# Performance work log

Hardware: AMD Instinct MI355X
Metric: run time of the kernel (lower is better)

The kernel has to match this reference:

```python
import jax, jax.numpy as jnp
import numpy as np

B, S, E, P, K, H = 32, 512, 1024, 256, 3, 8
KERNELS = 4  # conv repeated KERNELS times then averaged -> identical to a single conv


def setup_inputs() -> dict:
    key = jax.random.key(0)
    ks = jax.random.split(key, 8)
    sc = 0.02
    x = jax.random.normal(ks[0], (B, S, E), jnp.float32)
    # lengths must satisfy 3 <= l <= S-1 so slice [1:l+1] and conv length l-2 are valid
    seq_length = jax.random.randint(ks[1], (B,), 16, S - 1)
    proj_w = jax.random.normal(ks[2], (E, P), jnp.float32) * sc
    proj_b = jnp.zeros((P,), jnp.float32)
    conv_w = jax.random.normal(ks[3], (P, P, K), jnp.float32) * sc  # (out, in, width)
    conv_b = jnp.zeros((P,), jnp.float32)
    attn_w = jax.random.normal(ks[4], (P, H * S), jnp.float32) * sc
    attn_b = jnp.zeros((H * S,), jnp.float32)
    c1_w = jax.random.normal(ks[5], (P, P // 2), jnp.float32) * sc
    c1_b = jnp.zeros((P // 2,), jnp.float32)
    c2_w = jax.random.normal(ks[6], (P // 2, 2), jnp.float32) * sc
    c2_b = jnp.zeros((2,), jnp.float32)
    return dict(x=x, seq_length=seq_length, proj_w=proj_w, proj_b=proj_b,
                conv_w=conv_w, conv_b=conv_b, attn_w=attn_w, attn_b=attn_b,
                c1_w=c1_w, c1_b=c1_b, c2_w=c2_w, c2_b=c2_b)


def _forward(x, seq_length, proj_w, proj_b, conv_w, conv_b, attn_w, attn_b,
             c1_w, c1_b, c2_w, c2_b):
    # projection: (B,S,E) -> (B,S,P)
    proj = jnp.einsum('bse,ep->bsp', x, proj_w) + proj_b
    proj_pc = jnp.transpose(proj, (0, 2, 1))  # (B,P,S)
    # original convs each sample over slice [1:l+1]; conv is local, so conv the
    # full slice [1:] once and mask invalid tail positions per sample.
    conv = jax.lax.conv_general_dilated(
        proj_pc[:, :, 1:], conv_w, window_strides=(1,), padding='VALID',
        dimension_numbers=('NCH', 'OIH', 'NCH'))  # (B,P,S-K)
    conv = jax.nn.relu(conv + conv_b[None, :, None])
    # sum of KERNELS identical relu(conv) outputs divided by KERNELS == conv (identity)
    m = S - K  # conv output length over slice [1:]
    l = seq_length[:, None]  # (B,1)
    valid = jnp.arange(m)[None, :] < (l - (K - 1))  # output j valid iff j < l-2
    conv = jnp.where(valid[:, None, :], conv, 0.0)
    # pad: position 0 zero, conv outputs at 1..l-2, zeros after -> (B,P,S)
    rep_conv = jnp.zeros((B, P, S), conv.dtype).at[:, :, 1:1 + m].set(conv)
    rep_conv = jnp.transpose(rep_conv, (0, 2, 1))  # (B,S,P)
    # attention: logits (B,S,H*S), softmax over the FULL H*S axis (original dim=1)
    logits = jnp.einsum('bsp,pk->bsk', rep_conv, attn_w) + attn_b
    attn = jax.nn.softmax(logits, axis=-1).reshape(B, S, H, S)
    # per sample: mean over heads, sum over query rows -> weights over key pos q
    w = attn.sum(axis=(1, 2)) / H  # (B,S)
    rep_attn = jnp.einsum('bq,bqp->bp', w, rep_conv)  # (B,P)
    h = jnp.einsum('bp,ph->bh', rep_attn, c1_w) + c1_b
    h = jnp.where(h > 0, h, 0.01 * h)  # LeakyReLU(0.01)
    cls = jnp.einsum('bh,hc->bc', h, c2_w) + c2_b
    return jax.nn.softmax(cls, axis=-1)


def reference(x, seq_length, proj_w, proj_b, conv_w, conv_b, attn_w, attn_b,
              c1_w, c1_b, c2_w, c2_b):
    probs = _forward(x, seq_length, proj_w, proj_b, conv_w, conv_b,
                     attn_w, attn_b, c1_w, c1_b, c2_w, c2_b)
    return probs, jnp.argmax(probs, axis=1)
```

## Files before the change

kernel.cpp:

```cpp
#include <hip/hip_runtime.h>

#define B_ 32
#define S_ 512
#define E_ 1024
#define P_ 256
#define HH 8

typedef __attribute__((ext_vector_type(8))) short bf16x8;
typedef __attribute__((ext_vector_type(8))) unsigned short us8;
typedef __attribute__((ext_vector_type(4))) unsigned short us4;
typedef __attribute__((ext_vector_type(16))) float f32x16;

static __device__ __forceinline__ unsigned short f2bf(float f) {
  union { float f; unsigned int u; } v;
  v.f = f;
  unsigned int r = (v.u + 0x7FFFu + ((v.u >> 16) & 1u)) >> 16;
  return (unsigned short)r;
}
static __device__ __forceinline__ float bf2f(unsigned short u) {
  union { unsigned int u; float f; } v;
  v.u = ((unsigned int)u) << 16;
  return v.f;
}

__global__ __launch_bounds__(256) void k_wtT(const float* __restrict__ cw,
                                             unsigned short* __restrict__ wtT) {
  int o = blockIdx.x, k = blockIdx.y, i = threadIdx.x;
  wtT[o * 768 + k * 256 + i] = f2bf(cw[o * 768 + i * 3 + k]);
}

__global__ __launch_bounds__(256) void k_pwT(const float* __restrict__ pw,
                                             unsigned short* __restrict__ pwT) {
  __shared__ float T[32][33];
  int n0 = blockIdx.x * 32;
  int k0 = blockIdx.y * 32;
  int tx = threadIdx.x & 31, ty = threadIdx.x >> 5;
#pragma unroll
  for (int i = 0; i < 4; i++)
    T[ty + i * 8][tx] = pw[(k0 + ty + i * 8) * P_ + n0 + tx];
  __syncthreads();
#pragma unroll
  for (int i = 0; i < 4; i++)
    pwT[(size_t)(n0 + ty + i * 8) * E_ + k0 + tx] = f2bf(T[tx][ty + i * 8]);
}

__global__ __launch_bounds__(256) void k_awT(const float* __restrict__ aw,
                                             unsigned short* __restrict__ awT) {
  __shared__ float T[32][33];
  int j0 = blockIdx.x * 32;
  int k0 = blockIdx.y * 32;
  int tx = threadIdx.x & 31, ty = threadIdx.x >> 5;
#pragma unroll
  for (int i = 0; i < 4; i++)
    T[ty + i * 8][tx] = aw[(k0 + ty + i * 8) * 4096 + j0 + tx];
  __syncthreads();
#pragma unroll
  for (int i = 0; i < 4; i++)
    awT[(size_t)(j0 + ty + i * 8) * 256 + k0 + tx] = f2bf(T[tx][ty + i * 8]);
}

__global__ __launch_bounds__(256) void k_swz(const unsigned short* __restrict__ src,
                                             unsigned short* __restrict__ dst,
                                             int K, int NK) {
  int g = blockIdx.x, kc = blockIdx.y * 4 + (threadIdx.x >> 6);
  int l = threadIdx.x & 63;
  us8 v = *(const us8*)(src + (size_t)(g * 32 + (l & 31)) * K + kc * 16 + (l >> 5) * 8);
  *(us8*)(dst + ((size_t)g * NK + kc) * 512 + l * 8) = v;
}

__global__ __launch_bounds__(256) void k_zero(float* __restrict__ p) {
  p[blockIdx.x * 256 + threadIdx.x] = 0.f;
}

__global__ __launch_bounds__(256) void k_proj_mfma(const float* __restrict__ x,
                                                   const unsigned short* __restrict__ pwB,
                                                   const float* __restrict__ pb,
                                                   unsigned short* __restrict__ proj16) {
  __shared__ unsigned short As[16 * 64 * 8];
  const int m0 = blockIdx.x * 64;
  const int t = threadIdx.x;
  const int w = t >> 6, lane = t & 63, ln31 = lane & 31, kh = lane >> 5;
  const int c0 = w * 64;

  f32x16 acc00, acc01, acc10, acc11;
#pragma unroll
  for (int r = 0; r < 16; r++) { acc00[r] = 0.f; acc01[r] = 0.f; acc10[r] = 0.f; acc11[r] = 0.f; }

  const unsigned short* bp0 = pwB + (size_t)(2 * w) * 64 * 512 + lane * 8;
  const unsigned short* bp1 = bp0 + (size_t)64 * 512;

  for (int kc = 0; kc < E_; kc += 128) {
#pragma unroll
    for (int i = 0; i < 8; i++) {
      int c = t + i * 256;
      int row = c >> 5, pos = c & 31;
      float4 v = *(const float4*)(x + (size_t)(m0 + row) * E_ + kc + pos * 4);
      us4 h;
      h[0] = f2bf(v.x); h[1] = f2bf(v.y); h[2] = f2bf(v.z); h[3] = f2bf(v.w);
      *(us4*)&As[((pos >> 1) * 64 + row) * 8 + (pos & 1) * 4] = h;
    }
    __syncthreads();
    const int kcs = kc >> 4;
#pragma unroll
    for (int kk = 0; kk < 8; kk++) {
      bf16x8 a0 = *(const bf16x8*)&As[((2 * kk + kh) * 64 + ln31) * 8];
      bf16x8 a1 = *(const bf16x8*)&As[((2 * kk + kh) * 64 + 32 + ln31) * 8];
      bf16x8 b0 = *(const bf16x8*)(bp0 + (size_t)(kcs + kk) * 512);
      bf16x8 b1 = *(const bf16x8*)(bp1 + (size_t)(kcs + kk) * 512);
      acc00 = __builtin_amdgcn_mfma_f32_32x32x16_bf16(a0, b0, acc00, 0, 0, 0);
      acc01 = __builtin_amdgcn_mfma_f32_32x32x16_bf16(a0, b1, acc01, 0, 0, 0);
      acc10 = __builtin_amdgcn_mfma_f32_32x32x16_bf16(a1, b0, acc10, 0, 0, 0);
      acc11 = __builtin_amdgcn_mfma_f32_32x32x16_bf16(a1, b1, acc11, 0, 0, 0);
    }
    __syncthreads();
  }
  float pb0 = pb[c0 + ln31], pb1 = pb[c0 + 32 + ln31];
#pragma unroll
  for (int r = 0; r < 16; r++) {
    int rl = (r & 3) + 8 * (r >> 2) + 4 * kh;
    size_t g0 = (size_t)(m0 + rl) * P_;
    size_t g1 = (size_t)(m0 + 32 + rl) * P_;
    proj16[g0 + c0 + ln31]      = f2bf(acc00[r] + pb0);
    proj16[g0 + c0 + 32 + ln31] = f2bf(acc01[r] + pb1);
    proj16[g1 + c0 + ln31]      = f2bf(acc10[r] + pb0);
    proj16[g1 + c0 + 32 + ln31] = f2bf(acc11[r] + pb1);
  }
}

__global__ __launch_bounds__(256) void k_conv_mfma(const unsigned short* __restrict__ proj16,
                                                   const unsigned short* __restrict__ wtB,
                                                   const float* __restrict__ cb,
                                                   const int* __restrict__ seq,
                                                   unsigned short* __restrict__ rep16) {
  __shared__ unsigned short As[32 * 66 * 8];
  const int m0 = blockIdx.x * 64;
  const int bb = m0 >> 9, s0 = m0 & 511;
  const int t = threadIdx.x;
  const int w = t >> 6, lane = t & 63, ln31 = lane & 31, kh = lane >> 5;
  const int c0 = w * 64;

#pragma unroll
  for (int i = 0; i < 9; i++) {
    int c = t + i * 256;
    if (c < 2112) {
      int row = c >> 5, kk2 = c & 31;
      us8 v = {0, 0, 0, 0, 0, 0, 0, 0};
      if (s0 + row <= 511)
        v = *(const us8*)(proj16 + (size_t)(bb * S_ + s0 + row) * P_ + kk2 * 8);
      *(us8*)&As[(kk2 * 66 + row) * 8] = v;
    }
  }
  __syncthreads();

  f32x16 acc00, acc01, acc10, acc11;
#pragma unroll
  for (int r = 0; r < 16; r++) { acc00[r] = 0.f; acc01[r] = 0.f; acc10[r] = 0.f; acc11[r] = 0.f; }

  const unsigned short* bb0 = wtB + (size_t)(2 * w) * 48 * 512 + lane * 8;
  const unsigned short* bb1 = bb0 + (size_t)48 * 512;

#pragma unroll
  for (int k = 0; k < 3; k++) {
#pragma unroll
    for (int kk = 0; kk < 16; kk++) {
      bf16x8 a0 = *(const bf16x8*)&As[((2 * kk + kh) * 66 + k + ln31) * 8];
      bf16x8 a1 = *(const bf16x8*)&As[((2 * kk + kh) * 66 + k + 32 + ln31) * 8];
      bf16x8 b0 = *(const bf16x8*)(bb0 + (size_t)(k * 16 + kk) * 512);
      bf16x8 b1 = *(const bf16x8*)(bb1 + (size_t)(k * 16 + kk) * 512);
      acc00 = __builtin_amdgcn_mfma_f32_32x32x16_bf16(a0, b0, acc00, 0, 0, 0);
      acc01 = __builtin_amdgcn_mfma_f32_32x32x16_bf16(a0, b1, acc01, 0, 0, 0);
      acc10 = __builtin_amdgcn_mfma_f32_32x32x16_bf16(a1, b0, acc10, 0, 0, 0);
      acc11 = __builtin_amdgcn_mfma_f32_32x32x16_bf16(a1, b1, acc11, 0, 0, 0);
    }
  }

  int l = seq[bb];
  float cb0 = cb[c0 + ln31], cb1 = cb[c0 + 32 + ln31];
#pragma unroll
  for (int r = 0; r < 16; r++) {
    int rl = (r & 3) + 8 * (r >> 2) + 4 * kh;
    int s_a = s0 + rl, s_b = s0 + 32 + rl;
    float ma = (s_a >= 1 && s_a <= 509 && s_a < l - 1) ? 1.f : 0.f;
    float mb = (s_b >= 1 && s_b <= 509 && s_b < l - 1) ? 1.f : 0.f;
    size_t g0 = (size_t)(m0 + rl) * P_;
    size_t g1 = (size_t)(m0 + 32 + rl) * P_;
    rep16[g0 + c0 + ln31]      = f2bf(fmaxf(acc00[r] + cb0, 0.f) * ma);
    rep16[g0 + c0 + 32 + ln31] = f2bf(fmaxf(acc01[r] + cb1, 0.f) * ma);
    rep16[g1 + c0 + ln31]      = f2bf(fmaxf(acc10[r] + cb0, 0.f) * mb);
    rep16[g1 + c0 + 32 + ln31] = f2bf(fmaxf(acc11[r] + cb1, 0.f) * mb);
  }
}

__global__ __launch_bounds__(256) void k_attn_mfma(const unsigned short* __restrict__ rep16,
                                                   const unsigned short* __restrict__ awB,
                                                   const float* __restrict__ ab,
                                                   unsigned short* __restrict__ E16,
                                                   float* __restrict__ Z) {
  __shared__ unsigned short As[64][264];
  const int m0 = blockIdx.x * 64;
  const int q0 = blockIdx.y * 128;
  const int t = threadIdx.x;
  const int w = t >> 6;
  const int lane = t & 63;
  const int ln31 = lane & 31;
  const int kh = lane >> 5;
  const int khalf = kh * 8;

#pragma unroll
  for (int i = 0; i < 8; i++) {
    int flat = i * 256 + t;
    int r = flat >> 5;
    int g = (flat & 31) * 8;
    us8 v = *(const us8*)(rep16 + (size_t)(m0 + r) * 256 + g);
    *(us8*)&As[r][g] = v;
  }
  __syncthreads();

  const int qgidx = (q0 >> 5) + w;
  const int qcol = qgidx * 32 + ln31;
  const unsigned short* bg = awB + (size_t)qgidx * 16 * 512 + lane * 8;

  float ef0[16], ef1[16];
#pragma unroll
  for (int r = 0; r < 16; r++) { ef0[r] = 0.f; ef1[r] = 0.f; }

  for (int h = 0; h < HH; h++) {
    const unsigned short* bh = bg + (size_t)h * 16 * 16 * 512;
    f32x16 acc0, acc1;
#pragma unroll
    for (int r = 0; r < 16; r++) { acc0[r] = 0.f; acc1[r] = 0.f; }

#pragma unroll
    for (int kc = 0; kc < 16; kc++) {
      bf16x8 a0 = *(const bf16x8*)&As[ln31][kc * 16 + khalf];
      bf16x8 a1 = *(const bf16x8*)&As[32 + ln31][kc * 16 + khalf];
      bf16x8 b  = *(const bf16x8*)(bh + (size_t)kc * 512);
      acc0 = __builtin_amdgcn_mfma_f32_32x32x16_bf16(a0, b, acc0, 0, 0, 0);
      acc1 = __builtin_amdgcn_mfma_f32_32x32x16_bf16(a1, b, acc1, 0, 0, 0);
    }
    float bias = ab[h * 512 + qcol];
#pragma unroll
    for (int r = 0; r < 16; r++) {
      ef0[r] += __expf(acc0[r] + bias);
      ef1[r] += __expf(acc1[r] + bias);
    }
  }

#pragma unroll
  for (int r = 0; r < 16; r++) {
    int rl = (r & 3) + 8 * (r >> 2) + 4 * kh;
    E16[(size_t)(m0 + rl) * 512 + qcol]      = f2bf(ef0[r]);
    E16[(size_t)(m0 + 32 + rl) * 512 + qcol] = f2bf(ef1[r]);
  }

#pragma unroll
  for (int r = 0; r < 16; r++) {
    float z0 = ef0[r];
    float z1 = ef1[r];
#pragma unroll
    for (int st = 16; st >= 1; st >>= 1) {
      z0 += __shfl_xor(z0, st, 64);
      z1 += __shfl_xor(z1, st, 64);
    }
    if (ln31 == 0) {
      int rl = (r & 3) + 8 * (r >> 2) + 4 * kh;
      atomicAdd(&Z[m0 + rl], z0);
      atomicAdd(&Z[m0 + 32 + rl], z1);
    }
  }
}

__global__ __launch_bounds__(512) void k_w(const unsigned short* __restrict__ E16,
                                           const float* __restrict__ Z,
                                           float* __restrict__ wB) {
  __shared__ float rZ[64];
  int b = blockIdx.x, c = blockIdx.y, t = threadIdx.x;
  int s0 = c * 64;
  if (t < 64) rZ[t] = 1.0f / Z[b * 512 + s0 + t];
  __syncthreads();
  float acc = 0.f;
#pragma unroll 8
  for (int s = 0; s < 64; s++)
    acc += bf2f(E16[(size_t)(b * 512 + s0 + s) * 512 + t]) * rZ[s];
  atomicAdd(&wB[b * 512 + t], acc * (1.0f / HH));
}

__global__ __launch_bounds__(256) void k_final_a(const unsigned short* __restrict__ rep16,
                                                 const float* __restrict__ wB,
                                                 float* __restrict__ repA) {
  __shared__ float wS[64];
  int b = blockIdx.x, qc = blockIdx.y, t = threadIdx.x;
  if (t < 64) wS[t] = wB[b * 512 + qc * 64 + t];
  __syncthreads();
  float acc = 0.f;
  const unsigned short* base = rep16 + (size_t)(b * 512 + qc * 64) * 256 + t;
#pragma unroll 8
  for (int q = 0; q < 64; q++) acc += wS[q] * bf2f(base[(size_t)q * 256]);
  atomicAdd(&repA[b * 256 + t], acc);
}

__global__ __launch_bounds__(128) void k_final_b(const float* __restrict__ repA,
                                                 const float* __restrict__ c1w,
                                                 const float* __restrict__ c1b,
                                                 const float* __restrict__ c2w,
                                                 const float* __restrict__ c2b,
                                                 float* __restrict__ out) {
  __shared__ float hS[128];
  __shared__ float clsS[2];
  int b = blockIdx.x, t = threadIdx.x;
  float acc = c1b[t];
  for (int p = 0; p < 256; p++) acc += repA[b * 256 + p] * c1w[p * 128 + t];
  hS[t] = acc > 0.f ? acc : 0.01f * acc;
  __syncthreads();
  if (t < 2) {
    float a2 = c2b[t];
    for (int j = 0; j < 128; j++) a2 += hS[j] * c2w[j * 2 + t];
    clsS[t] = a2;
  }
  __syncthreads();
  if (t == 0) {
    float c0 = clsS[0], c1 = clsS[1];
    float m = fmaxf(c0, c1);
    float e0 = __expf(c0 - m), e1 = __expf(c1 - m);
    float inv = 1.0f / (e0 + e1);
    float p0 = e0 * inv, p1 = e1 * inv;
    out[b * 2 + 0] = p0;
    out[b * 2 + 1] = p1;
    out[B_ * 2 + b] = (p1 > p0) ? 1.0f : 0.0f;
  }
}

extern "C" void kernel_launch(void* const* d_in, const int* in_sizes, int n_in,
                              void* d_out, int out_size, void* d_ws, size_t ws_size,
                              hipStream_t stream) {
  const float* x   = (const float*)d_in[0];
  const int*   seq = (const int*)d_in[1];
  const float* pw  = (const float*)d_in[2];
  const float* pb  = (const float*)d_in[3];
  const float* cw  = (const float*)d_in[4];
  const float* cb  = (const float*)d_in[5];
  const float* aw  = (const float*)d_in[6];
  const float* ab  = (const float*)d_in[7];
  const float* c1w = (const float*)d_in[8];
  const float* c1b = (const float*)d_in[9];
  const float* c2w = (const float*)d_in[10];
  const float* c2b = (const float*)d_in[11];
  float* out = (float*)d_out;

  char* ws = (char*)d_ws;
  unsigned short* proj16 = (unsigned short*)(ws);
  unsigned short* E16    = (unsigned short*)(ws);
  unsigned short* rep16  = (unsigned short*)(ws + (size_t)16777216);
  unsigned short* pwT    = (unsigned short*)(ws + (size_t)25165824);
  unsigned short* wtT    = (unsigned short*)(ws + (size_t)25690112);
  unsigned short* awT    = (unsigned short*)(ws + (size_t)26083328);
  float*          Z      = (float*)(ws + (size_t)28180480);
  float*          wB     = (float*)(ws + (size_t)28246016);
  float*          repA   = (float*)(ws + (size_t)28311552);
  unsigned short* awB    = (unsigned short*)(ws + (size_t)28377088);
  unsigned short* pwB    = (unsigned short*)(ws + (size_t)30474240);
  unsigned short* wtB    = (unsigned short*)(ws + (size_t)30998528);

  k_zero<<<160, 256, 0, stream>>>(Z);
  k_wtT<<<dim3(256, 3), 256, 0, stream>>>(cw, wtT);
  k_pwT<<<dim3(8, 32), 256, 0, stream>>>(pw, pwT);
  k_awT<<<dim3(128, 8), 256, 0, stream>>>(aw, awT);
  k_swz<<<dim3(128, 4), 256, 0, stream>>>(awT, awB, 256, 16);
  k_swz<<<dim3(8, 16), 256, 0, stream>>>(pwT, pwB, 1024, 64);
  k_swz<<<dim3(8, 12), 256, 0, stream>>>(wtT, wtB, 768, 48);

  k_proj_mfma<<<256, 256, 0, stream>>>(x, pwB, pb, proj16);
  k_conv_mfma<<<256, 256, 0, stream>>>(proj16, wtB, cb, seq, rep16);
  k_attn_mfma<<<dim3(256, 4), 256, 0, stream>>>(rep16, awB, ab, E16, Z);
  k_w<<<dim3(32, 8), 512, 0, stream>>>(E16, Z, wB);
  k_final_a<<<dim3(32, 8), 256, 0, stream>>>(rep16, wB, repA);
  k_final_b<<<32, 128, 0, stream>>>(repA, c1w, c1b, c2w, c2b, out);
}
```

Measured before the change: 252.2 us.

## Pre-swizzle conv output and hold attention A operands in registers

Adds a swizzle pass that lays out the bf16 conv output (rep16) in MFMA operand order (repF). The attention kernel then loads all A fragments for its 64 rows straight into registers instead of staging them through shared memory with a barrier. It also sets launch_bounds occupancy to 2 and stops the head loop from unrolling. The cost is an extra kernel launch with a full read and write of rep16, plus heavy register pressure from 32 bf16x8 A fragments per thread, which could cause spills or lower occupancy.

After: 249.5 us. Within noise of the previous version (-1.0%).

```diff
diff --git a/kernel.cpp b/kernel.cpp
--- a/kernel.cpp
+++ b/kernel.cpp
@@ -191,12 +191,11 @@
   }
 }
 
-__global__ __launch_bounds__(256) void k_attn_mfma(const unsigned short* __restrict__ rep16,
-                                                   const unsigned short* __restrict__ awB,
-                                                   const float* __restrict__ ab,
-                                                   unsigned short* __restrict__ E16,
-                                                   float* __restrict__ Z) {
-  __shared__ unsigned short As[64][264];
+__global__ __launch_bounds__(256, 2) void k_attn_mfma(const unsigned short* __restrict__ repF,
+                                                      const unsigned short* __restrict__ awB,
+                                                      const float* __restrict__ ab,
+                                                      unsigned short* __restrict__ E16,
+                                                      float* __restrict__ Z) {
   const int m0 = blockIdx.x * 64;
   const int q0 = blockIdx.y * 128;
   const int t = threadIdx.x;
@@ -204,39 +203,36 @@
   const int lane = t & 63;
   const int ln31 = lane & 31;
   const int kh = lane >> 5;
-  const int khalf = kh * 8;
-
-#pragma unroll
-  for (int i = 0; i < 8; i++) {
-    int flat = i * 256 + t;
-    int r = flat >> 5;
-    int g = (flat & 31) * 8;
-    us8 v = *(const us8*)(rep16 + (size_t)(m0 + r) * 256 + g);
-    *(us8*)&As[r][g] = v;
-  }
-  __syncthreads();
+
+  bf16x8 ar0[16], ar1[16];
+  {
+    const unsigned short* abase = repF + ((size_t)(m0 >> 5) * 16) * 512 + lane * 8;
+#pragma unroll
+    for (int kc = 0; kc < 16; kc++) {
+      ar0[kc] = *(const bf16x8*)(abase + (size_t)kc * 512);
+      ar1[kc] = *(const bf16x8*)(abase + (size_t)(16 + kc) * 512);
+    }
+  }
 
   const int qgidx = (q0 >> 5) + w;
   const int qcol = qgidx * 32 + ln31;
-  const unsigned short* bg = awB + (size_t)qgidx * 16 * 512 + lane * 8;
 
   float ef0[16], ef1[16];
 #pragma unroll
   for (int r = 0; r < 16; r++) { ef0[r] = 0.f; ef1[r] = 0.f; }
 
+#pragma unroll 1
   for (int h = 0; h < HH; h++) {
-    const unsigned short* bh = bg + (size_t)h * 16 * 16 * 512;
+    const unsigned short* bh = awB + ((size_t)(h * 16 + qgidx) * 16) * 512 + lane * 8;
     f32x16 acc0, acc1;
 #pragma unroll
     for (int r = 0; r < 16; r++) { acc0[r] = 0.f; acc1[r] = 0.f; }
 
 #pragma unroll
     for (int kc = 0; kc < 16; kc++) {
-      bf16x8 a0 = *(const bf16x8*)&As[ln31][kc * 16 + khalf];
-      bf16x8 a1 = *(const bf16x8*)&As[32 + ln31][kc * 16 + khalf];
-      bf16x8 b  = *(const bf16x8*)(bh + (size_t)kc * 512);
-      acc0 = __builtin_amdgcn_mfma_f32_32x32x16_bf16(a0, b, acc0, 0, 0, 0);
-      acc1 = __builtin_amdgcn_mfma_f32_32x32x16_bf16(a1, b, acc1, 0, 0, 0);
+      bf16x8 b = *(const bf16x8*)(bh + (size_t)kc * 512);
+      acc0 = __builtin_amdgcn_mfma_f32_32x32x16_bf16(ar0[kc], b, acc0, 0, 0, 0);
+      acc1 = __builtin_amdgcn_mfma_f32_32x32x16_bf16(ar1[kc], b, acc1, 0, 0, 0);
     }
     float bias = ab[h * 512 + qcol];
 #pragma unroll
@@ -360,6 +356,7 @@
   unsigned short* awB    = (unsigned short*)(ws + (size_t)28377088);
   unsigned short* pwB    = (unsigned short*)(ws + (size_t)30474240);
   unsigned short* wtB    = (unsigned short*)(ws + (size_t)30998528);
+  unsigned short* repF   = (unsigned short*)(ws + (size_t)31391744);
 
   k_zero<<<160, 256, 0, stream>>>(Z);
   k_wtT<<<dim3(256, 3), 256, 0, stream>>>(cw, wtT);
@@ -371,7 +368,8 @@
 
   k_proj_mfma<<<256, 256, 0, stream>>>(x, pwB, pb, proj16);
   k_conv_mfma<<<256, 256, 0, stream>>>(proj16, wtB, cb, seq, rep16);
-  k_attn_mfma<<<dim3(256, 4), 256, 0, stream>>>(rep16, awB, ab, E16, Z);
+  k_swz<<<dim3(512, 4), 256, 0, stream>>>(rep16, repF, 256, 16);
+  k_attn_mfma<<<dim3(256, 4), 256, 0, stream>>>(repF, awB, ab, E16, Z);
   k_w<<<dim3(32, 8), 512, 0, stream>>>(E16, Z, wB);
   k_final_a<<<dim3(32, 8), 256, 0, stream>>>(rep16, wB, repA);
   k_final_b<<<32, 128, 0, stream>>>(repA, c1w, c1b, c2w, c2b, out);
```
